# Kernel optimization log

Hardware: AMD Instinct MI355X
Metric: run time of the kernel (lower is better)

Reference implementation:

```python
import jax, jax.numpy as jnp
import numpy as np

N_NODES = 50000
N_EDGES = 640000
N_GRAPHS = 64
IN_DIM, HID, OUT_DIM = 128, 256, 4


def gcn_conv(x, src, dst, W, b, n_nodes):
    """PyG GCNConv: linear transform, then sym-normalized aggregation with self-loops."""
    h = x @ W  # [N, out]
    deg = jnp.zeros((n_nodes,), h.dtype).at[dst].add(1.0) + 1.0  # +1 self-loop
    dinv = jax.lax.rsqrt(deg)  # deg >= 1 always
    norm = dinv[src] * dinv[dst]  # [E]
    msg = h[src] * norm[:, None]  # [E, out]  gather + scale
    agg = jax.ops.segment_sum(msg, dst, num_segments=n_nodes)  # scatter-add
    agg = agg + h * (dinv * dinv)[:, None]  # self-loop contribution
    return agg + b


def global_mean_pool(x, batch, num_graphs):
    s = jax.ops.segment_sum(x, batch, num_segments=num_graphs)
    cnt = jax.ops.segment_sum(jnp.ones((x.shape[0],), x.dtype), batch, num_segments=num_graphs)
    return s / jnp.clip(cnt, 1.0)[:, None]


def setup_inputs() -> dict:
    key = jax.random.key(0)
    ks = jax.random.split(key, 8)
    x = jax.random.normal(ks[0], (N_NODES, IN_DIM), jnp.float32)
    src = jax.random.randint(ks[1], (N_EDGES,), 0, N_NODES, jnp.int64 if jax.config.jax_enable_x64 else jnp.int32)
    dst = jax.random.randint(ks[2], (N_EDGES,), 0, N_NODES, src.dtype)
    batch = jnp.sort(jax.random.randint(ks[3], (N_NODES,), 0, N_GRAPHS, src.dtype))
    W1 = jax.random.normal(ks[4], (IN_DIM, HID), jnp.float32) * (1.0 / np.sqrt(IN_DIM))
    b1 = jnp.zeros((HID,), jnp.float32)
    W2 = jax.random.normal(ks[5], (HID, HID // 2), jnp.float32) * (1.0 / np.sqrt(HID))
    b2 = jnp.zeros((HID // 2,), jnp.float32)
    Wfc = jax.random.normal(ks[6], (HID // 2, OUT_DIM), jnp.float32) * (1.0 / np.sqrt(HID // 2))
    bfc = jnp.zeros((OUT_DIM,), jnp.float32)
    return {"x": x, "src": src, "dst": dst, "batch": batch,
            "W1": W1, "b1": b1, "W2": W2, "b2": b2, "Wfc": Wfc, "bfc": bfc}


def reference(x, src, dst, batch, W1, b1, W2, b2, Wfc, bfc):
    n = x.shape[0]
    h = jax.nn.relu(gcn_conv(x, src, dst, W1, b1, n))   # dropout is identity at inference
    h = jax.nn.relu(gcn_conv(h, src, dst, W2, b2, n))
    g = global_mean_pool(h, batch, N_GRAPHS)            # [G, HID//2]
    return g @ Wfc + bfc                                # [G, OUT_DIM]
```

## Files before the change

kernel.cpp:

```cpp
#include <hip/hip_runtime.h>


constexpr int IN_DIM  = 128;
constexpr int HID     = 256;
constexpr int HID2    = 128;
constexpr int OUT_DIM = 4;
constexpr int NGRAPH  = 64;

typedef __attribute__((ext_vector_type(8))) short bf16x8;
typedef __attribute__((ext_vector_type(4))) float f32x4;

__device__ __forceinline__ short f2bf(float f) {
    union { float f; unsigned u; } v; v.f = f;
    unsigned r = v.u + 0x7fff + ((v.u >> 16) & 1);
    return (short)(r >> 16);
}
__device__ __forceinline__ float bf2f(short s) {
    union { unsigned u; float f; } v; v.u = ((unsigned)(unsigned short)s) << 16;
    return v.f;
}


__global__ void wprep_all_kernel(const float* __restrict__ W1, short* __restrict__ W1th,
                                 short* __restrict__ W1tl,
                                 const float* __restrict__ W2, short* __restrict__ W2th,
                                 short* __restrict__ W2tl,
                                 int* __restrict__ count, float* __restrict__ pool, int N) {
    int i = blockIdx.x * blockDim.x + threadIdx.x;
    if (i < IN_DIM * HID) {
        int k = i / HID, n = i % HID;
        float w = W1[i];
        short h = f2bf(w);
        W1th[n * IN_DIM + k] = h;
        W1tl[n * IN_DIM + k] = f2bf(w - bf2f(h));
    }
    if (i < HID * HID2) {
        int k = i / HID2, n = i % HID2;
        float w = W2[i];
        short h = f2bf(w);
        W2th[n * HID + k] = h;
        W2tl[n * HID + k] = f2bf(w - bf2f(h));
    }
    if (i < N) count[i] = 0;
    if (i < NGRAPH * HID2) pool[i] = 0.f;
}


__global__ void hist_kernel(const int* __restrict__ dst, int* __restrict__ count,
                            ushort* __restrict__ rank, int E) {
    int i = blockIdx.x * blockDim.x + threadIdx.x;
    if (i < E) rank[i] = (ushort)atomicAdd(&count[dst[i]], 1);
}

__global__ void scan1_kernel(const int* __restrict__ count, int* __restrict__ bsums, int N) {
    __shared__ int s[256];
    int t = threadIdx.x, i = blockIdx.x * 256 + t;
    int v = (i < N) ? count[i] : 0;
    s[t] = v; __syncthreads();
    for (int o = 1; o < 256; o <<= 1) {
        int x = (t >= o) ? s[t - o] : 0;
        __syncthreads(); s[t] += x; __syncthreads();
    }
    if (t == 255) bsums[blockIdx.x] = s[255];
}

__global__ void scan3_kernel(const int* __restrict__ count, const int* __restrict__ bsums,
                             int* __restrict__ rowptr, float* __restrict__ dinv,
                             int N, int E, int nb) {
    __shared__ int sb[256];
    __shared__ int s[256];
    int t = threadIdx.x, i = blockIdx.x * 256 + t;
    int bv = (t < nb) ? bsums[t] : 0;
    sb[t] = bv; __syncthreads();
    for (int o = 1; o < 256; o <<= 1) {
        int x = (t >= o) ? sb[t - o] : 0;
        __syncthreads(); sb[t] += x; __syncthreads();
    }
    int myex = (blockIdx.x == 0) ? 0 : sb[blockIdx.x - 1];
    int v = (i < N) ? count[i] : 0;
    s[t] = v; __syncthreads();
    for (int o = 1; o < 256; o <<= 1) {
        int x = (t >= o) ? s[t - o] : 0;
        __syncthreads(); s[t] += x; __syncthreads();
    }
    if (i < N) {
        rowptr[i] = myex + s[t] - v;
        dinv[i] = rsqrtf((float)v + 1.0f);
        if (i == 0) rowptr[N] = E;
    }
}

__global__ void scatter_scale_kernel(const int* __restrict__ src, const int* __restrict__ dst,
                                     const ushort* __restrict__ rank,
                                     const int* __restrict__ rowptr, ushort* __restrict__ csr,
                                     const float* __restrict__ x, const float* __restrict__ dinv,
                                     ushort* __restrict__ xb, int E, int total2) {
    int i = blockIdx.x * blockDim.x + threadIdx.x;
    if (i < E) {
        int p = rowptr[dst[i]] + (int)rank[i];
        csr[p] = (ushort)src[i];
    }
    if (i < total2) {
        float d = dinv[i >> 6];
        float2 v = ((const float2*)x)[i];
        ushort2 o;
        o.x = (ushort)f2bf(v.x * d);
        o.y = (ushort)f2bf(v.y * d);
        ((ushort2*)xb)[i] = o;
    }
}


__launch_bounds__(256, 4)
__global__ void mlp_fused_kernel(const short* __restrict__ A,
                                 const short* __restrict__ W1h, const short* __restrict__ W1l,
                                 const float* __restrict__ b1,
                                 const short* __restrict__ W2h, const short* __restrict__ W2l,
                                 const float* __restrict__ dinv,
                                 short* __restrict__ Cb, int M) {
    __shared__ __align__(16) short L[12288 + 6144];
    short* A1 = L;
    short* A0 = L + 12288;
    __shared__ float dinv_s[48];

    const int tid  = threadIdx.x;
    const int w    = tid >> 6;
    const int lane = tid & 63;
    const int l15  = lane & 15;
    const int kq8  = (lane >> 4) * 8;
    const int row0 = blockIdx.x * 48;
    const int flane = ((lane >> 2) | ((lane & 3) << 4)) & 63;

    {
        bf16x8 stg[3];
#pragma unroll
        for (int j = 0; j < 3; ++j) {
            int s = w * 3 + j;
            int m = s >> 2, ks = s & 3;
            int rr = row0 + m * 16 + l15; if (rr >= M) rr = M - 1;
            stg[j] = *(const bf16x8*)(A + (size_t)rr * IN_DIM + ks * 32 + kq8);
        }
#pragma unroll
        for (int j = 0; j < 3; ++j)
            *(bf16x8*)&A0[(w * 3 + j) * 512 + lane * 8] = stg[j];
    }
    if (tid < 48) { int r = row0 + tid; dinv_s[tid] = dinv[r < M ? r : M - 1]; }
    __syncthreads();

    f32x4 acc1[3][4];
#pragma unroll
    for (int m = 0; m < 3; ++m)
#pragma unroll
        for (int n = 0; n < 4; ++n) acc1[m][n] = f32x4{0.f, 0.f, 0.f, 0.f};

    const short* w1hp = W1h + (size_t)(w * 64 + l15) * IN_DIM + kq8;
    const short* w1lp = W1l + (size_t)(w * 64 + l15) * IN_DIM + kq8;
#pragma unroll
    for (int ks = 0; ks < 4; ++ks) {
        bf16x8 af[3], bh[4], bl[4];
#pragma unroll
        for (int m = 0; m < 3; ++m) af[m] = *(const bf16x8*)&A0[(m * 4 + ks) * 512 + lane * 8];
#pragma unroll
        for (int n = 0; n < 4; ++n) {
            bh[n] = *(const bf16x8*)(w1hp + (size_t)(n * 16) * IN_DIM + ks * 32);
            bl[n] = *(const bf16x8*)(w1lp + (size_t)(n * 16) * IN_DIM + ks * 32);
        }
#pragma unroll
        for (int m = 0; m < 3; ++m)
#pragma unroll
            for (int n = 0; n < 4; ++n) {
                acc1[m][n] = __builtin_amdgcn_mfma_f32_16x16x32_bf16(af[m], bh[n], acc1[m][n], 0, 0, 0);
                acc1[m][n] = __builtin_amdgcn_mfma_f32_16x16x32_bf16(af[m], bl[n], acc1[m][n], 0, 0, 0);
            }
    }

#pragma unroll
    for (int n = 0; n < 4; ++n) {
        int c  = w * 64 + n * 16 + l15;
        float bv = b1[c];
        int kst = c >> 5;
        int q  = (c >> 3) & 3;
        int e  = c & 7;
#pragma unroll
        for (int m = 0; m < 3; ++m)
#pragma unroll
            for (int r4 = 0; r4 < 4; ++r4) {
                int rl = (lane >> 4) * 4 + r4;
                int d  = rl + 16 * q;
                int fd = ((d >> 2) | ((d & 3) << 4)) & 63;
                float v = fmaxf(acc1[m][n][r4] + bv, 0.f);
                A1[(m * 8 + kst) * 512 + fd * 8 + e] = f2bf(v);
            }
    }
    __syncthreads();

    f32x4 acc2[3][2];
#pragma unroll
    for (int m = 0; m < 3; ++m)
#pragma unroll
        for (int n = 0; n < 2; ++n) acc2[m][n] = f32x4{0.f, 0.f, 0.f, 0.f};

    const short* w2hp = W2h + (size_t)(w * 32 + l15) * HID + kq8;
    const short* w2lp = W2l + (size_t)(w * 32 + l15) * HID + kq8;
#pragma unroll
    for (int ks = 0; ks < 8; ++ks) {
        bf16x8 af[3], bh[2], bl[2];
#pragma unroll
        for (int m = 0; m < 3; ++m) af[m] = *(const bf16x8*)&A1[(m * 8 + ks) * 512 + flane * 8];
#pragma unroll
        for (int n = 0; n < 2; ++n) {
            bh[n] = *(const bf16x8*)(w2hp + (size_t)(n * 16) * HID + ks * 32);
            bl[n] = *(const bf16x8*)(w2lp + (size_t)(n * 16) * HID + ks * 32);
        }
#pragma unroll
        for (int m = 0; m < 3; ++m)
#pragma unroll
            for (int n = 0; n < 2; ++n) {
                acc2[m][n] = __builtin_amdgcn_mfma_f32_16x16x32_bf16(af[m], bh[n], acc2[m][n], 0, 0, 0);
                acc2[m][n] = __builtin_amdgcn_mfma_f32_16x16x32_bf16(af[m], bl[n], acc2[m][n], 0, 0, 0);
            }
    }
    __syncthreads();

    short* T = A1;
#pragma unroll
    for (int n = 0; n < 2; ++n) {
        int c = w * 32 + n * 16 + l15;
#pragma unroll
        for (int m = 0; m < 3; ++m)
#pragma unroll
            for (int r4 = 0; r4 < 4; ++r4) {
                int r = m * 16 + (lane >> 4) * 4 + r4;
                T[r * 132 + c] = f2bf(acc2[m][n][r4] * dinv_s[r]);
            }
    }
    __syncthreads();
#pragma unroll
    for (int it = 0; it < 3; ++it) {
        int chunk = it * 256 + tid;
        int lr = chunk >> 4;
        int lc = (chunk & 15) * 8;
        int gr = row0 + lr;
        if (gr < M)
            *(bf16x8*)(Cb + (size_t)gr * HID2 + lc) = *(const bf16x8*)&T[lr * 132 + lc];
    }
}


template <bool POOL>
__launch_bounds__(256)
__global__ void agg_group_kernel(const ushort* __restrict__ hb, const float* __restrict__ dinv,
                                 const int* __restrict__ rowptr, const ushort* __restrict__ csr,
                                 const float* __restrict__ bias,
                                 short* __restrict__ oh,
                                 const int* __restrict__ batch, float* __restrict__ pool,
                                 int N) {
    __shared__ float pacc[16][128];
    __shared__ int   sgid[16];

    const int tid  = threadIdx.x;
    const int li   = tid & 15;
    const int nib  = tid >> 4;
    const int node = blockIdx.x * 16 + nib;
    const bool valid = node < N;
    if (!POOL && !valid) return;
    const int cw = valid ? node : N - 1;

    const int lo = rowptr[cw], hi = rowptr[cw + 1];
    const float dd = dinv[cw];

    float a[8];
    {
        bf16x8 sv = *(const bf16x8*)(hb + ((size_t)cw << 7) + (li << 3));
#pragma unroll
        for (int d = 0; d < 8; ++d) a[d] = bf2f(sv[d]);
    }

    const ushort* hsl = hb + (li << 3);

    for (int base = lo; base < hi; base += 16) {
        int cnt = min(16, hi - base);
        int sidx = (int)csr[base + (li < cnt ? li : cnt - 1)];
        bf16x8 p[8], q[8];
#pragma unroll
        for (int u = 0; u < 8; ++u) {
            int s = __shfl(sidx, u < cnt ? u : cnt - 1, 16);
            p[u] = *(const bf16x8*)(hsl + ((size_t)s << 7));
        }
#pragma unroll
        for (int u = 0; u < 8; ++u) {
            int e = 8 + u;
            int s = __shfl(sidx, e < cnt ? e : cnt - 1, 16);
            q[u] = *(const bf16x8*)(hsl + ((size_t)s << 7));
        }
#pragma unroll
        for (int u = 0; u < 8; ++u) {
            bool v = u < cnt;
#pragma unroll
            for (int d = 0; d < 8; ++d) a[d] += v ? bf2f(p[u][d]) : 0.f;
        }
#pragma unroll
        for (int u = 0; u < 8; ++u) {
            bool v = 8 + u < cnt;
#pragma unroll
            for (int d = 0; d < 8; ++d) a[d] += v ? bf2f(q[u][d]) : 0.f;
        }
    }

#pragma unroll
    for (int d = 0; d < 8; ++d) a[d] *= dd;

    if (!POOL) {
        if (valid) {
            bf16x8 o;
#pragma unroll
            for (int d = 0; d < 8; ++d) o[d] = f2bf(a[d]);
            *(bf16x8*)&oh[(size_t)node * 128 + li * 8] = o;
        }
        return;
    }

    {
        float4 b0 = ((const float4*)bias)[li * 2];
        float4 b1 = ((const float4*)bias)[li * 2 + 1];
        a[0] = fmaxf(a[0] + b0.x, 0.f); a[1] = fmaxf(a[1] + b0.y, 0.f);
        a[2] = fmaxf(a[2] + b0.z, 0.f); a[3] = fmaxf(a[3] + b0.w, 0.f);
        a[4] = fmaxf(a[4] + b1.x, 0.f); a[5] = fmaxf(a[5] + b1.y, 0.f);
        a[6] = fmaxf(a[6] + b1.z, 0.f); a[7] = fmaxf(a[7] + b1.w, 0.f);
    }
    if (li == 0) sgid[nib] = valid ? batch[node] : -1;
#pragma unroll
    for (int d = 0; d < 8; ++d) pacc[nib][li * 8 + d] = a[d];
    __syncthreads();
    if (tid < 128) {
        int c = tid;
        int cur = sgid[0];
        float run = 0.f;
#pragma unroll 1
        for (int w = 0; w < 16; ++w) {
            int gi = sgid[w];
            if (gi < 0) break;
            if (gi != cur) { atomicAdd(&pool[cur * HID2 + c], run); run = 0.f; cur = gi; }
            run += pacc[w][c];
        }
        atomicAdd(&pool[cur * HID2 + c], run);
    }
}


__device__ __forceinline__ int lower_bound_i(const int* __restrict__ a, int n, int key) {
    int lo = 0, hi = n;
    while (lo < hi) {
        int mid = (lo + hi) >> 1;
        if (a[mid] < key) lo = mid + 1; else hi = mid;
    }
    return lo;
}

__global__ void fc_kernel(const float* __restrict__ pool, const int* __restrict__ batch,
                          const float* __restrict__ Wfc, const float* __restrict__ bfc,
                          float* __restrict__ out, int N) {
    int t = threadIdx.x;
    int g = t >> 2, o = t & 3;
    int lo = lower_bound_i(batch, N, g);
    int hi = lower_bound_i(batch, N, g + 1);
    float acc = 0.f;
#pragma unroll 8
    for (int c = 0; c < HID2; ++c)
        acc = fmaf(pool[g * HID2 + c], Wfc[c * OUT_DIM + o], acc);
    float inv = 1.0f / fmaxf((float)(hi - lo), 1.0f);
    out[g * OUT_DIM + o] = acc * inv + bfc[o];
}

extern "C" void kernel_launch(void* const* d_in, const int* in_sizes, int n_in,
                              void* d_out, int out_size, void* d_ws, size_t ws_size,
                              hipStream_t stream) {
    const float* x   = (const float*)d_in[0];
    const int* src   = (const int*)d_in[1];
    const int* dst   = (const int*)d_in[2];
    const int* batch = (const int*)d_in[3];
    const float* W1  = (const float*)d_in[4];
    const float* b1  = (const float*)d_in[5];
    const float* W2  = (const float*)d_in[6];
    const float* b2  = (const float*)d_in[7];
    const float* Wfc = (const float*)d_in[8];
    const float* bfc = (const float*)d_in[9];
    float* out = (float*)d_out;

    const int N = in_sizes[0] / IN_DIM;
    const int E = in_sizes[1];
    const int NB = (N + 255) / 256;
    const int GA = (N + 15) / 16;
    const int GM = (N + 47) / 48;

    char* ws = (char*)d_ws;
    size_t off = 0;
    auto alloc = [&](size_t bytes) {
        char* p = ws + off;
        off = (off + bytes + 255) & ~(size_t)255;
        return p;
    };
    float*  dinv   = (float*) alloc((size_t)N * 4);
    int*    count  = (int*)   alloc((size_t)N * 4);
    int*    rowptr = (int*)   alloc((size_t)(N + 1) * 4);
    int*    bsums  = (int*)   alloc(256 * 4);
    ushort* rank   = (ushort*)alloc((size_t)E * 2);
    ushort* csr    = (ushort*)alloc((size_t)E * 2);
    short*  W1th   = (short*) alloc((size_t)IN_DIM * HID * 2);
    short*  W1tl   = (short*) alloc((size_t)IN_DIM * HID * 2);
    short*  W2th   = (short*) alloc((size_t)HID * HID2 * 2);
    short*  W2tl   = (short*) alloc((size_t)HID * HID2 * 2);
    ushort* xb     = (ushort*)alloc((size_t)N * IN_DIM * 2);
    short*  axb    = (short*) alloc((size_t)N * IN_DIM * 2);
    float*  pool   = (float*) alloc((size_t)NGRAPH * HID2 * 4);
    ushort* h2b = xb;

    wprep_all_kernel<<<(max(IN_DIM * HID, N) + 255) / 256, 256, 0, stream>>>(
        W1, W1th, W1tl, W2, W2th, W2tl, count, pool, N);

    hist_kernel<<<(E + 255) / 256, 256, 0, stream>>>(dst, count, rank, E);
    scan1_kernel<<<NB, 256, 0, stream>>>(count, bsums, N);
    scan3_kernel<<<NB, 256, 0, stream>>>(count, bsums, rowptr, dinv, N, E, NB);
    scatter_scale_kernel<<<(N * 64 + 255) / 256, 256, 0, stream>>>(
        src, dst, rank, rowptr, csr, x, dinv, xb, E, N * 64);

    agg_group_kernel<false><<<GA, 256, 0, stream>>>(
        xb, dinv, rowptr, csr, nullptr, axb, nullptr, nullptr, N);

    mlp_fused_kernel<<<GM, 256, 0, stream>>>(
        axb, W1th, W1tl, b1, W2th, W2tl, dinv, (short*)h2b, N);

    agg_group_kernel<true><<<GA, 256, 0, stream>>>(
        h2b, dinv, rowptr, csr, b2, nullptr, batch, pool, N);

    fc_kernel<<<1, NGRAPH * OUT_DIM, 0, stream>>>(pool, batch, Wfc, bfc, out, N);
}
```

Baseline: 247.1 us.

## Preload MLP weight fragments into registers ahead of LDS staging and barriers

The fused MLP kernel now loads all W1 hi/lo fragments into registers before staging the A tile, and all W2 fragments before the barrier that precedes the second GEMM. This lets global weight loads overlap the LDS staging and barrier waits instead of sitting inside the MFMA loops. The launch bound drops from 4 to 2 blocks per SM to allow the extra registers, and the flane swizzle on A1 writes and reads is removed. Lower occupancy and unswizzled LDS access may add bank conflicts or hurt latency hiding.

After: 248.9 us. No clear change (+0.7%).

```diff
diff --git a/kernel.cpp b/kernel.cpp
--- a/kernel.cpp
+++ b/kernel.cpp
@@ -111,7 +111,7 @@
 }
 
 
-__launch_bounds__(256, 4)
+__launch_bounds__(256, 2)
 __global__ void mlp_fused_kernel(const short* __restrict__ A,
                                  const short* __restrict__ W1h, const short* __restrict__ W1l,
                                  const float* __restrict__ b1,
@@ -129,7 +129,17 @@
     const int l15  = lane & 15;
     const int kq8  = (lane >> 4) * 8;
     const int row0 = blockIdx.x * 48;
-    const int flane = ((lane >> 2) | ((lane & 3) << 4)) & 63;
+
+    const short* w1hp = W1h + (size_t)(w * 64 + l15) * IN_DIM + kq8;
+    const short* w1lp = W1l + (size_t)(w * 64 + l15) * IN_DIM + kq8;
+    bf16x8 wh1[4][4], wl1[4][4];
+#pragma unroll
+    for (int ks = 0; ks < 4; ++ks)
+#pragma unroll
+        for (int n = 0; n < 4; ++n) {
+            wh1[ks][n] = *(const bf16x8*)(w1hp + (size_t)(n * 16) * IN_DIM + ks * 32);
+            wl1[ks][n] = *(const bf16x8*)(w1lp + (size_t)(n * 16) * IN_DIM + ks * 32);
+        }
 
     {
         bf16x8 stg[3];
@@ -153,24 +163,17 @@
 #pragma unroll
         for (int n = 0; n < 4; ++n) acc1[m][n] = f32x4{0.f, 0.f, 0.f, 0.f};
 
-    const short* w1hp = W1h + (size_t)(w * 64 + l15) * IN_DIM + kq8;
-    const short* w1lp = W1l + (size_t)(w * 64 + l15) * IN_DIM + kq8;
 #pragma unroll
     for (int ks = 0; ks < 4; ++ks) {
-        bf16x8 af[3], bh[4], bl[4];
+        bf16x8 af[3];
 #pragma unroll
         for (int m = 0; m < 3; ++m) af[m] = *(const bf16x8*)&A0[(m * 4 + ks) * 512 + lane * 8];
 #pragma unroll
-        for (int n = 0; n < 4; ++n) {
-            bh[n] = *(const bf16x8*)(w1hp + (size_t)(n * 16) * IN_DIM + ks * 32);
-            bl[n] = *(const bf16x8*)(w1lp + (size_t)(n * 16) * IN_DIM + ks * 32);
-        }
-#pragma unroll
         for (int m = 0; m < 3; ++m)
 #pragma unroll
             for (int n = 0; n < 4; ++n) {
-                acc1[m][n] = __builtin_amdgcn_mfma_f32_16x16x32_bf16(af[m], bh[n], acc1[m][n], 0, 0, 0);
-                acc1[m][n] = __builtin_amdgcn_mfma_f32_16x16x32_bf16(af[m], bl[n], acc1[m][n], 0, 0, 0);
+                acc1[m][n] = __builtin_amdgcn_mfma_f32_16x16x32_bf16(af[m], wh1[ks][n], acc1[m][n], 0, 0, 0);
+                acc1[m][n] = __builtin_amdgcn_mfma_f32_16x16x32_bf16(af[m], wl1[ks][n], acc1[m][n], 0, 0, 0);
             }
     }
 
@@ -187,37 +190,40 @@
             for (int r4 = 0; r4 < 4; ++r4) {
                 int rl = (lane >> 4) * 4 + r4;
                 int d  = rl + 16 * q;
-                int fd = ((d >> 2) | ((d & 3) << 4)) & 63;
                 float v = fmaxf(acc1[m][n][r4] + bv, 0.f);
-                A1[(m * 8 + kst) * 512 + fd * 8 + e] = f2bf(v);
+                A1[(m * 8 + kst) * 512 + d * 8 + e] = f2bf(v);
             }
     }
-    __syncthreads();
-
-    f32x4 acc2[3][2];
-#pragma unroll
-    for (int m = 0; m < 3; ++m)
-#pragma unroll
-        for (int n = 0; n < 2; ++n) acc2[m][n] = f32x4{0.f, 0.f, 0.f, 0.f};
 
     const short* w2hp = W2h + (size_t)(w * 32 + l15) * HID + kq8;
     const short* w2lp = W2l + (size_t)(w * 32 + l15) * HID + kq8;
+    bf16x8 wh2[8][2], wl2[8][2];
+#pragma unroll
+    for (int ks = 0; ks < 8; ++ks)
+#pragma unroll
+        for (int n = 0; n < 2; ++n) {
+            wh2[ks][n] = *(const bf16x8*)(w2hp + (size_t)(n * 16) * HID + ks * 32);
+            wl2[ks][n] = *(const bf16x8*)(w2lp + (size_t)(n * 16) * HID + ks * 32);
+        }
+    __syncthreads();
+
+    f32x4 acc2[3][2];
+#pragma unroll
+    for (int m = 0; m < 3; ++m)
+#pragma unroll
+        for (int n = 0; n < 2; ++n) acc2[m][n] = f32x4{0.f, 0.f, 0.f, 0.f};
+
 #pragma unroll
     for (int ks = 0; ks < 8; ++ks) {
-        bf16x8 af[3], bh[2], bl[2];
-#pragma unroll
-        for (int m = 0; m < 3; ++m) af[m] = *(const bf16x8*)&A1[(m * 8 + ks) * 512 + flane * 8];
-#pragma unroll
-        for (int n = 0; n < 2; ++n) {
-            bh[n] = *(const bf16x8*)(w2hp + (size_t)(n * 16) * HID + ks * 32);
-            bl[n] = *(const bf16x8*)(w2lp + (size_t)(n * 16) * HID + ks * 32);
-        }
+        bf16x8 af[3];
+#pragma unroll
+        for (int m = 0; m < 3; ++m) af[m] = *(const bf16x8*)&A1[(m * 8 + ks) * 512 + lane * 8];
 #pragma unroll
         for (int m = 0; m < 3; ++m)
 #pragma unroll
             for (int n = 0; n < 2; ++n) {
-                acc2[m][n] = __builtin_amdgcn_mfma_f32_16x16x32_bf16(af[m], bh[n], acc2[m][n], 0, 0, 0);
-                acc2[m][n] = __builtin_amdgcn_mfma_f32_16x16x32_bf16(af[m], bl[n], acc2[m][n], 0, 0, 0);
+                acc2[m][n] = __builtin_amdgcn_mfma_f32_16x16x32_bf16(af[m], wh2[ks][n], acc2[m][n], 0, 0, 0);
+                acc2[m][n] = __builtin_amdgcn_mfma_f32_16x16x32_bf16(af[m], wl2[ks][n], acc2[m][n], 0, 0, 0);
             }
     }
     __syncthreads();
```
